# Performance work log

Measured on AMD Instinct MI355X. Metric: run time of the kernel, lower is better.

The kernel has to match this reference:

```python
import jax, jax.numpy as jnp
import numpy as np

N = 3072
FEAT = 128
E = 24576


def setup_inputs() -> dict:
    key = jax.random.key(0)
    k1, k2, k3, k4 = jax.random.split(key, 4)
    x = jax.random.normal(k1, (N, FEAT), dtype=jnp.float32)
    edge_index = jax.random.randint(k2, (2, E), 0, N, dtype=jnp.int32)
    batch = jnp.zeros((N,), dtype=jnp.int32)
    # lin: Linear(2*FEAT, 1)
    w = jax.random.normal(k3, (2 * FEAT,), dtype=jnp.float32) / np.sqrt(2 * FEAT)
    b = jax.random.normal(k4, (), dtype=jnp.float32) * 0.01
    return {"x": x, "edge_index": edge_index, "batch": batch, "w": w, "b": b}


def _cc_labels(adj):
    """Connected-component labels via min-label propagation + pointer jumping.
    Labels equal the minimum node index of each component, so ranking them by
    value reproduces scipy's first-occurrence component ordering."""
    n = adj.shape[0]
    adj = jax.lax.stop_gradient(adj)

    def body(state):
        labels, _ = state
        neigh = jnp.where(adj > 0, labels[None, :], n).min(axis=1)  # [n]
        new = jnp.minimum(labels, neigh)
        new = jnp.minimum(new, new[new])  # pointer jumping
        return new, jnp.any(new != labels)

    labels, _ = jax.lax.while_loop(lambda s: s[1], body,
                                   (jnp.arange(n), jnp.array(True)))
    return labels


def reference(x, edge_index, batch, w, b):
    n, f = x.shape
    idx = jnp.arange(n)
    src, dst = edge_index[0], edge_index[1]
    # undirected: duplicate each edge in both directions (coalesce in the
    # original dedups; dense scatter-set below is equivalent since duplicate
    # (u,v) edges get identical scores)
    s2 = jnp.concatenate([src, dst])
    d2 = jnp.concatenate([dst, src])
    # per-edge raw score: lin(concat(x[u], x[v]))  ->  tanh
    e = jnp.tanh(x[s2] @ w[:f] + x[d2] @ w[f:] + b)  # [2E]

    zero = jnp.zeros((n, n), dtype=x.dtype)
    A = zero.at[s2, d2].set(1.0).at[idx, idx].set(0.0)   # self-loops removed
    S = zero.at[s2, d2].set(e).at[idx, idx].set(0.0)
    contract = (e > 0.0).astype(x.dtype)                 # tanh -> threshold 0
    A_c = zero.at[s2, d2].max(contract).at[idx, idx].set(0.0)

    labels = _cc_labels(A_c)                             # min-node-index labels
    roots = (labels == idx).astype(jnp.int32)
    cluster = (jnp.cumsum(roots) - 1)[labels]            # consecutive 0..K-1
    C = jax.nn.one_hot(cluster, n, dtype=x.dtype)        # [n, n] (padded to n)

    single = (A_c.sum(axis=1) + A_c.sum(axis=0)) == 0    # isolated under contraction
    S = S.at[idx, idx].set(single.astype(x.dtype))

    X_new = (S @ C).T @ x                                # [n(padK), f]
    A_new = (C.T @ A @ C).at[idx, idx].set(0.0)          # dense coarsened adjacency
    new_batch = jnp.zeros((n,), dtype=batch.dtype).at[cluster].max(batch)
    return X_new, A_new, new_batch, cluster
```

## Files before the change

kernel.cpp:

```cpp
#include <hip/hip_runtime.h>
#include <math.h>

#define N 3072
#define FEAT 128
#define NE 24576
#define PSTRIDE 64
#define DOTB 768
#define OUTZ4 2458368
#define ZB3 608
#define GATB 192
#define RESCAP 4096

__device__ __forceinline__ void wave_agg_add(bool valid, int key, float val,
                                             float* base, int stride, int off) {
    int lane = threadIdx.x & 63;
    unsigned long long active = __ballot(valid ? 1 : 0);
    while (active) {
        int leader = __ffsll(active) - 1;
        int lkey = __shfl(key, leader);
        bool mine = valid && (key == lkey);
        unsigned long long grp = __ballot(mine ? 1 : 0);
        float v = mine ? val : 0.0f;
        #pragma unroll
        for (int o = 32; o; o >>= 1) v += __shfl_xor(v, o);
        if (lane == leader)
            atomicAdd(&base[(size_t)lkey * stride + off], v);
        active &= ~grp;
    }
}

__global__ void k_init(const float* __restrict__ x, const float* __restrict__ w,
                       float* __restrict__ a, float* __restrict__ c,
                       float4* __restrict__ zws) {
    int b = blockIdx.x, t = threadIdx.x;
    if (b < DOTB) {
        int node = b * 4 + (t >> 6);
        int lane = t & 63;
        const float* xi = x + node * FEAT;
        float pa = xi[lane] * w[lane] + xi[lane + 64] * w[lane + 64];
        float pc = xi[lane] * w[FEAT + lane] + xi[lane + 64] * w[FEAT + lane + 64];
        for (int off = 32; off; off >>= 1) {
            pa += __shfl_down(pa, off);
            pc += __shfl_down(pc, off);
        }
        if (lane == 0) { a[node] = pa; c[node] = pc; }
    } else {
        float4 z = {0.f, 0.f, 0.f, 0.f};
        #pragma unroll
        for (int k = 0; k < 6; ++k) zws[k * 256 + t] = z;
    }
}

__global__ void k_edge_pairs(const int* __restrict__ ei, const float* __restrict__ a,
                             const float* __restrict__ c, const float* __restrict__ bb,
                             unsigned* __restrict__ ep, int* __restrict__ notsingle,
                             int* __restrict__ pcnt, unsigned long long* __restrict__ ptab) {
    int t = blockIdx.x * blockDim.x + threadIdx.x;
    if (t >= NE) return;
    int u = ei[t], v = ei[NE + t];
    unsigned wpk = (unsigned)u | ((unsigned)v << 12);
    if (u != v) {
        float b = bb[0];
        float su = a[u] + c[v] + b;
        float sv = a[v] + c[u] + b;
        unsigned fu = (su > 0.f) ? 1u : 0u;
        unsigned fv = (sv > 0.f) ? 1u : 0u;
        wpk |= (fu << 24) | (fv << 25);
        if (fu | fv) { notsingle[u] = 1; notsingle[v] = 1; }
        float eu = tanhf(su);
        int sl = atomicAdd(&pcnt[v], 1);
        if (sl < PSTRIDE)
            ptab[(size_t)v * PSTRIDE + sl] =
                ((unsigned long long)__float_as_uint(eu) << 32) | (unsigned)u;
        float ev2 = tanhf(sv);
        sl = atomicAdd(&pcnt[u], 1);
        if (sl < PSTRIDE)
            ptab[(size_t)u * PSTRIDE + sl] =
                ((unsigned long long)__float_as_uint(ev2) << 32) | (unsigned)v;
    }
    ep[t] = wpk;
}

__global__ void __launch_bounds__(1024)
k_prop_gather(const unsigned* __restrict__ ep, const float* __restrict__ x,
              const int* __restrict__ pcnt, const unsigned long long* __restrict__ ptab,
              const int* __restrict__ notsingle, float* __restrict__ y,
              unsigned long long* __restrict__ qmask, int* __restrict__ cluster,
              float* __restrict__ out_cluster, float4* __restrict__ zout) {
    __shared__ int lab[N];
    __shared__ unsigned Vw[N / 32];
    __shared__ unsigned res[RESCAP];
    __shared__ unsigned short rnodes[N];
    __shared__ int ssum[1024];
    __shared__ unsigned short rk[N];
    __shared__ int sh_p[16 * 64];
    __shared__ int flag, rescnt, rncnt;
    int t = threadIdx.x, blk = blockIdx.x;
    int wv = t >> 6, lane = t & 63;
    if (blk == 0) {
        if (t < N / 32) Vw[t] = (t == 0) ? 1u : 0u;
        if (t == 0) { rescnt = 0; rncnt = 0; }
        unsigned act = 0x00FFFFFFu;
        for (;;) {
            __syncthreads();
            if (t == 0) flag = 0;
            __syncthreads();
            unsigned rem = act;
            while (rem) {
                int j = __ffs(rem) - 1;
                rem &= rem - 1;
                unsigned wpk = ep[t + j * 1024];
                if (!(wpk & 0x3000000u)) { act &= ~(1u << j); continue; }
                int u = wpk & 0xFFF, v = (wpk >> 12) & 0xFFF;
                unsigned pu = (Vw[u >> 5] >> (u & 31)) & 1u;
                unsigned pv = (Vw[v >> 5] >> (v & 31)) & 1u;
                if ((wpk & (1u << 24)) && pv && !pu) {
                    atomicOr(&Vw[u >> 5], 1u << (u & 31)); pu = 1; flag = 1;
                }
                if ((wpk & (1u << 25)) && pu && !pv) {
                    atomicOr(&Vw[v >> 5], 1u << (v & 31)); pv = 1; flag = 1;
                }
                bool done = (pu || !(wpk & (1u << 24))) && (pv || !(wpk & (1u << 25)));
                if (done) act &= ~(1u << j);
            }
            __syncthreads();
            if (!flag) break;
        }
        unsigned rem = act;
        while (rem) {
            int j = __ffs(rem) - 1;
            rem &= rem - 1;
            unsigned wpk = ep[t + j * 1024];
            int u = wpk & 0xFFF, v = (wpk >> 12) & 0xFFF;
            unsigned pu = (Vw[u >> 5] >> (u & 31)) & 1u;
            unsigned pv = (Vw[v >> 5] >> (v & 31)) & 1u;
            if ((wpk & (1u << 24)) && !pu) {
                int pos = atomicAdd(&rescnt, 1);
                if (pos < RESCAP) res[pos] = (unsigned)u | ((unsigned)v << 12);
            }
            if ((wpk & (1u << 25)) && !pv) {
                int pos = atomicAdd(&rescnt, 1);
                if (pos < RESCAP) res[pos] = (unsigned)v | ((unsigned)u << 12);
            }
        }
        for (int i = t; i < N; i += 1024) {
            unsigned inV = (Vw[i >> 5] >> (i & 31)) & 1u;
            lab[i] = inV ? 0 : i;
            if (!inV) {
                int pos = atomicAdd(&rncnt, 1);
                rnodes[pos] = (unsigned short)i;
            }
        }
        __syncthreads();
        int nres = rescnt < RESCAP ? rescnt : RESCAP;
        bool ovf = (rescnt > RESCAP);
        int nrn = rncnt;
        for (;;) {
            __syncthreads();
            if (t == 0) flag = 0;
            __syncthreads();
            if (!ovf) {
                for (int k = t; k < nres; k += 1024) {
                    unsigned w2 = res[k];
                    int p = w2 & 0xFFF, q = (w2 >> 12) & 0xFFF;
                    int lq = lab[q];
                    if (lq < lab[p]) { atomicMin(&lab[p], lq); flag = 1; }
                }
                for (int k = t; k < nrn; k += 1024) {
                    int i = rnodes[k];
                    int m = lab[i];
                    int mm = lab[m];
                    while (mm < m) { m = mm; mm = lab[m]; }
                    if (m < lab[i]) { atomicMin(&lab[i], m); flag = 1; }
                }
            } else {
                for (int j = 0; j < 24; ++j) {
                    unsigned wpk = ep[t + j * 1024];
                    int u = wpk & 0xFFF, v = (wpk >> 12) & 0xFFF;
                    if (wpk & (1u << 24)) {
                        int lv = lab[v];
                        if (lv < lab[u]) { atomicMin(&lab[u], lv); flag = 1; }
                    }
                    if (wpk & (1u << 25)) {
                        int lu = lab[u];
                        if (lu < lab[v]) { atomicMin(&lab[v], lu); flag = 1; }
                    }
                }
                for (int i = t; i < N; i += 1024) {
                    int m = lab[i];
                    if (m == 0) continue;
                    int mm = lab[m];
                    while (mm < m) { m = mm; mm = lab[m]; }
                    if (m < lab[i]) { atomicMin(&lab[i], m); flag = 1; }
                }
            }
            __syncthreads();
            if (!flag) break;
        }
        int i0 = 3 * t;
        int r0 = (lab[i0] == i0);
        int r1 = (lab[i0 + 1] == i0 + 1);
        int r2 = (lab[i0 + 2] == i0 + 2);
        int s = r0 + r1 + r2;
        ssum[t] = s;
        __syncthreads();
        for (int off = 1; off < 1024; off <<= 1) {
            int val = (t >= off) ? ssum[t - off] : 0;
            __syncthreads();
            ssum[t] += val;
            __syncthreads();
        }
        int run = ssum[t] - s;
        run += r0; rk[i0]     = (unsigned short)(run - 1);
        run += r1; rk[i0 + 1] = (unsigned short)(run - 1);
        run += r2; rk[i0 + 2] = (unsigned short)(run - 1);
        __syncthreads();
        for (int j = t; j < N; j += 1024) {
            int cl = rk[lab[j]];
            cluster[j] = cl;
            out_cluster[j] = (float)cl;
        }
    } else if (blk <= GATB) {
        int q = (blk - 1) * 16 + wv;
        int cnt = pcnt[q]; if (cnt > PSTRIDE) cnt = PSTRIDE;
        const unsigned long long* row = ptab + (size_t)q * PSTRIDE;
        int myp = -1 - lane;
        float mye = 0.f;
        if (lane < cnt) {
            unsigned long long s = row[lane];
            myp = (int)(s & 0xFFFFFFFFu);
            mye = __uint_as_float((unsigned)(s >> 32));
        }
        sh_p[wv * 64 + lane] = myp;
        bool dup = false;
        for (int j = 0; j < lane && !dup; ++j)
            dup = (sh_p[wv * 64 + j] == myp);
        bool valid = (lane < cnt) && !dup;
        unsigned long long m = __ballot(valid ? 1 : 0);
        if (lane == 0) qmask[q] = m;
        float acc0 = 0.f, acc1 = 0.f;
        for (int j = 0; j < cnt; ++j) {
            if (!((m >> j) & 1ull)) continue;
            int p = __shfl(myp, j);
            float e = __shfl(mye, j);
            const float* xp = x + p * FEAT;
            acc0 += e * xp[lane];
            acc1 += e * xp[lane + 64];
        }
        if (!notsingle[q]) {
            const float* xq = x + q * FEAT;
            acc0 += xq[lane];
            acc1 += xq[lane + 64];
        }
        float* yq = y + q * FEAT;
        yq[lane] = acc0;
        yq[lane + 64] = acc1;
    } else {
        float4 z = {0.f, 0.f, 0.f, 0.f};
        int base = (blk - GATB - 1) * 4096;
        #pragma unroll
        for (int k = 0; k < 4; ++k) {
            int idx = base + k * 1024 + t;
            if (idx < OUTZ4) zout[idx] = z;
        }
    }
}

__global__ void k_reduce_anew(const float* __restrict__ y, const int* __restrict__ cluster,
                              const int* __restrict__ pcnt,
                              const unsigned long long* __restrict__ ptab,
                              const unsigned long long* __restrict__ qmask,
                              float* __restrict__ Xnew, float* __restrict__ Anew) {
    int gid = blockIdx.x * blockDim.x + threadIdx.x;
    int wid = gid >> 6, lane = gid & 63;
    if (wid < 6144) {
        int f = wid & (FEAT - 1);
        int chunk = wid >> 7;
        int q = chunk * 64 + lane;
        wave_agg_add(true, cluster[q], y[q * FEAT + f], Xnew, FEAT, f);
    } else {
        int q = wid - 6144;
        int cnt = pcnt[q]; if (cnt > PSTRIDE) cnt = PSTRIDE;
        unsigned long long m = qmask[q];
        bool valid = (lane < cnt) && ((m >> lane) & 1ull);
        int p = 0;
        if (valid) p = (int)(ptab[(size_t)q * PSTRIDE + lane] & 0xFFFFFFFFu);
        int cq = cluster[q];
        int cp = valid ? cluster[p] : 0;
        valid = valid && (cp != cq);
        wave_agg_add(valid, cp * N + cq, 1.0f, Anew, 1, 0);
    }
}

extern "C" void kernel_launch(void* const* d_in, const int* in_sizes, int n_in,
                              void* d_out, int out_size, void* d_ws, size_t ws_size,
                              hipStream_t stream) {
    const float* x  = (const float*)d_in[0];
    const int*   ei = (const int*)d_in[1];
    const float* w  = (const float*)d_in[3];
    const float* bb = (const float*)d_in[4];

    char* ws = (char*)d_ws;
    size_t off = 0;
    int* pcnt     = (int*)(ws + off);      off += (size_t)N * 4;
    int* notsing  = (int*)(ws + off);      off += (size_t)N * 4;
    float* a      = (float*)(ws + off);    off += (size_t)N * 4;
    float* c      = (float*)(ws + off);    off += (size_t)N * 4;
    int* cluster  = (int*)(ws + off);      off += (size_t)N * 4;
    unsigned* ep  = (unsigned*)(ws + off); off += (size_t)NE * 4;
    unsigned long long* qmask = (unsigned long long*)(ws + off); off += (size_t)N * 8;
    float* y      = (float*)(ws + off);    off += (size_t)N * FEAT * 4;
    unsigned long long* ptab = (unsigned long long*)(ws + off); off += (size_t)N * PSTRIDE * 8;

    float* Xnew        = (float*)d_out;
    float* Anew        = Xnew + (size_t)N * FEAT;
    float* out_cluster = Anew + (size_t)N * N + N;

    k_init<<<DOTB + 1, 256, 0, stream>>>(x, w, a, c, (float4*)pcnt);
    k_edge_pairs<<<NE / 256, 256, 0, stream>>>(ei, a, c, bb, ep, notsing, pcnt, ptab);
    k_prop_gather<<<1 + GATB + ZB3, 1024, 0, stream>>>(ep, x, pcnt, ptab, notsing, y,
                                                       qmask, cluster, out_cluster,
                                                       (float4*)d_out);
    k_reduce_anew<<<(9216 * 64) / 1024, 1024, 0, stream>>>(y, cluster, pcnt, ptab,
                                                           qmask, Xnew, Anew);
}
```

Baseline: 134.0 us.

## Fuse gather and reduction kernels using in-kernel spin-wait barriers

Merges the feature-gather and the Xnew/Anew scatter-reduction into a single launch. Gather blocks keep their per-node aggregates in registers and wait on global counters until the cluster labels are computed and the output buffers are zeroed. Before issuing atomics they combine same-cluster rows within the block through shared memory. This removes the y and qmask round-trip through global memory and one kernel launch. In exchange it relies on all 770 blocks of 1024 threads being co-resident, which risks deadlock or serialization if they are not.

Result: slower. 387.4 us (+189.2%).

```diff
diff --git a/kernel.cpp b/kernel.cpp
--- a/kernel.cpp
+++ b/kernel.cpp
@@ -6,9 +6,9 @@
 #define NE 24576
 #define PSTRIDE 64
 #define DOTB 768
-#define OUTZ4 2458368
-#define ZB3 608
 #define GATB 192
+#define AZ4 2360064
+#define AZB 577
 #define RESCAP 4096
 
 __device__ __forceinline__ void wave_agg_add(bool valid, int key, float val,
@@ -29,6 +29,10 @@
     }
 }
 
+__device__ __forceinline__ int ctrl_ld(const int* p) {
+    return __hip_atomic_load(p, __ATOMIC_RELAXED, __HIP_MEMORY_SCOPE_AGENT);
+}
+
 __global__ void k_init(const float* __restrict__ x, const float* __restrict__ w,
                        float* __restrict__ a, float* __restrict__ c,
                        float4* __restrict__ zws) {
@@ -47,7 +51,10 @@
     } else {
         float4 z = {0.f, 0.f, 0.f, 0.f};
         #pragma unroll
-        for (int k = 0; k < 6; ++k) zws[k * 256 + t] = z;
+        for (int k = 0; k < 7; ++k) {
+            int idx = k * 256 + t;
+            if (idx < 1540) zws[idx] = z;
+        }
     }
 }
 
@@ -82,11 +89,11 @@
 }
 
 __global__ void __launch_bounds__(1024)
-k_prop_gather(const unsigned* __restrict__ ep, const float* __restrict__ x,
-              const int* __restrict__ pcnt, const unsigned long long* __restrict__ ptab,
-              const int* __restrict__ notsingle, float* __restrict__ y,
-              unsigned long long* __restrict__ qmask, int* __restrict__ cluster,
-              float* __restrict__ out_cluster, float4* __restrict__ zout) {
+k_pgr2(const unsigned* __restrict__ ep, const float* __restrict__ x,
+       const int* __restrict__ pcnt, const unsigned long long* __restrict__ ptab,
+       const int* __restrict__ notsingle, int* __restrict__ cluster,
+       float* __restrict__ out_cluster, float* __restrict__ Xnew,
+       float* __restrict__ Anew, int* __restrict__ ctrl) {
     __shared__ int lab[N];
     __shared__ unsigned Vw[N / 32];
     __shared__ unsigned res[RESCAP];
@@ -94,6 +101,9 @@
     __shared__ int ssum[1024];
     __shared__ unsigned short rk[N];
     __shared__ int sh_p[16 * 64];
+    __shared__ int sh_cq[16];
+    __shared__ float sh_a0[16 * 64];
+    __shared__ float sh_a1[16 * 64];
     __shared__ int flag, rescnt, rncnt;
     int t = threadIdx.x, blk = blockIdx.x;
     int wv = t >> 6, lane = t & 63;
@@ -220,7 +230,17 @@
             cluster[j] = cl;
             out_cluster[j] = (float)cl;
         }
+        __syncthreads();
+        __threadfence();
+        if (t == 0) atomicAdd(&ctrl[2], 1);
     } else if (blk <= GATB) {
+        {
+            float4 z = {0.f, 0.f, 0.f, 0.f};
+            if (t < 512) ((float4*)Xnew)[(blk - 1) * 512 + t] = z;
+            __syncthreads();
+            __threadfence();
+            if (t == 0) atomicAdd(&ctrl[4], 1);
+        }
         int q = (blk - 1) * 16 + wv;
         int cnt = pcnt[q]; if (cnt > PSTRIDE) cnt = PSTRIDE;
         const unsigned long long* row = ptab + (size_t)q * PSTRIDE;
@@ -237,7 +257,6 @@
             dup = (sh_p[wv * 64 + j] == myp);
         bool valid = (lane < cnt) && !dup;
         unsigned long long m = __ballot(valid ? 1 : 0);
-        if (lane == 0) qmask[q] = m;
         float acc0 = 0.f, acc1 = 0.f;
         for (int j = 0; j < cnt; ++j) {
             if (!((m >> j) & 1ull)) continue;
@@ -252,43 +271,43 @@
             acc0 += xq[lane];
             acc1 += xq[lane + 64];
         }
-        float* yq = y + q * FEAT;
-        yq[lane] = acc0;
-        yq[lane + 64] = acc1;
+        if (t == 0) {
+            while (ctrl_ld(&ctrl[4]) < GATB) __builtin_amdgcn_s_sleep(2);
+            while (ctrl_ld(&ctrl[2]) < 1)    __builtin_amdgcn_s_sleep(2);
+            while (ctrl_ld(&ctrl[3]) < AZB)  __builtin_amdgcn_s_sleep(2);
+        }
+        __syncthreads();
+        __threadfence();
+        int cq = cluster[q];
+        if (lane == 0) sh_cq[wv] = cq;
+        sh_a0[wv * 64 + lane] = acc0;
+        sh_a1[wv * 64 + lane] = acc1;
+        __syncthreads();
+        bool leader = true;
+        for (int j = 0; j < wv; ++j)
+            if (sh_cq[j] == cq) leader = false;
+        if (leader) {
+            float s0 = acc0, s1 = acc1;
+            for (int j = wv + 1; j < 16; ++j)
+                if (sh_cq[j] == cq) { s0 += sh_a0[j * 64 + lane]; s1 += sh_a1[j * 64 + lane]; }
+            atomicAdd(&Xnew[cq * FEAT + lane], s0);
+            atomicAdd(&Xnew[cq * FEAT + 64 + lane], s1);
+        }
+        int cp = valid ? cluster[myp] : 0;
+        bool av = valid && (cp != cq);
+        wave_agg_add(av, cp * N + cq, 1.0f, Anew, 1, 0);
     } else {
         float4 z = {0.f, 0.f, 0.f, 0.f};
+        float4* az = (float4*)Anew;
         int base = (blk - GATB - 1) * 4096;
         #pragma unroll
         for (int k = 0; k < 4; ++k) {
             int idx = base + k * 1024 + t;
-            if (idx < OUTZ4) zout[idx] = z;
-        }
-    }
-}
-
-__global__ void k_reduce_anew(const float* __restrict__ y, const int* __restrict__ cluster,
-                              const int* __restrict__ pcnt,
-                              const unsigned long long* __restrict__ ptab,
-                              const unsigned long long* __restrict__ qmask,
-                              float* __restrict__ Xnew, float* __restrict__ Anew) {
-    int gid = blockIdx.x * blockDim.x + threadIdx.x;
-    int wid = gid >> 6, lane = gid & 63;
-    if (wid < 6144) {
-        int f = wid & (FEAT - 1);
-        int chunk = wid >> 7;
-        int q = chunk * 64 + lane;
-        wave_agg_add(true, cluster[q], y[q * FEAT + f], Xnew, FEAT, f);
-    } else {
-        int q = wid - 6144;
-        int cnt = pcnt[q]; if (cnt > PSTRIDE) cnt = PSTRIDE;
-        unsigned long long m = qmask[q];
-        bool valid = (lane < cnt) && ((m >> lane) & 1ull);
-        int p = 0;
-        if (valid) p = (int)(ptab[(size_t)q * PSTRIDE + lane] & 0xFFFFFFFFu);
-        int cq = cluster[q];
-        int cp = valid ? cluster[p] : 0;
-        valid = valid && (cp != cq);
-        wave_agg_add(valid, cp * N + cq, 1.0f, Anew, 1, 0);
+            if (idx < AZ4) az[idx] = z;
+        }
+        __syncthreads();
+        __threadfence();
+        if (t == 0) atomicAdd(&ctrl[3], 1);
     }
 }
 
@@ -302,25 +321,21 @@
 
     char* ws = (char*)d_ws;
     size_t off = 0;
+    int* ctrl     = (int*)(ws + off);      off += 64;
     int* pcnt     = (int*)(ws + off);      off += (size_t)N * 4;
     int* notsing  = (int*)(ws + off);      off += (size_t)N * 4;
     float* a      = (float*)(ws + off);    off += (size_t)N * 4;
     float* c      = (float*)(ws + off);    off += (size_t)N * 4;
     int* cluster  = (int*)(ws + off);      off += (size_t)N * 4;
     unsigned* ep  = (unsigned*)(ws + off); off += (size_t)NE * 4;
-    unsigned long long* qmask = (unsigned long long*)(ws + off); off += (size_t)N * 8;
-    float* y      = (float*)(ws + off);    off += (size_t)N * FEAT * 4;
     unsigned long long* ptab = (unsigned long long*)(ws + off); off += (size_t)N * PSTRIDE * 8;
 
     float* Xnew        = (float*)d_out;
     float* Anew        = Xnew + (size_t)N * FEAT;
     float* out_cluster = Anew + (size_t)N * N + N;
 
-    k_init<<<DOTB + 1, 256, 0, stream>>>(x, w, a, c, (float4*)pcnt);
+    k_init<<<DOTB + 1, 256, 0, stream>>>(x, w, a, c, (float4*)ctrl);
     k_edge_pairs<<<NE / 256, 256, 0, stream>>>(ei, a, c, bb, ep, notsing, pcnt, ptab);
-    k_prop_gather<<<1 + GATB + ZB3, 1024, 0, stream>>>(ep, x, pcnt, ptab, notsing, y,
-                                                       qmask, cluster, out_cluster,
-                                                       (float4*)d_out);
-    k_reduce_anew<<<(9216 * 64) / 1024, 1024, 0, stream>>>(y, cluster, pcnt, ptab,
-                                                           qmask, Xnew, Anew);
-}
+    k_pgr2<<<1 + GATB + AZB, 1024, 0, stream>>>(ep, x, pcnt, ptab, notsing,
+                                                cluster, out_cluster, Xnew, Anew, ctrl);
+}
```

## Fuse edge, propagation and reduction kernels into persistent kernel with grid barriers

Applied to the files above, without the earlier changes.

Merges the edge-pair, propagation/gather and reduce kernels into one 256-block persistent kernel separated by software grid barriers. The output zeroing moves into the init kernel, which also clears the barrier counters. This removes two kernel launches and their gaps. In exchange, every block now waits at the barriers for the single-block label propagation, and correctness relies on all 256 blocks of 1024 threads being resident at the same time.

New measurement: 177.4 us. 1.32x slower.

```diff
diff --git a/kernel.cpp b/kernel.cpp
--- a/kernel.cpp
+++ b/kernel.cpp
@@ -6,9 +6,9 @@
 #define NE 24576
 #define PSTRIDE 64
 #define DOTB 768
-#define OUTZ4 2458368
-#define ZB3 608
-#define GATB 192
+#define OZ4 2459136
+#define OZB 2402
+#define NBLK 256
 #define RESCAP 4096
 
 __device__ __forceinline__ void wave_agg_add(bool valid, int key, float val,
@@ -29,9 +29,30 @@
     }
 }
 
+__device__ __forceinline__ void gsync(int* bar, int* lgen) {
+    __syncthreads();
+    if (threadIdx.x == 0) {
+        __threadfence();
+        int g = ++(*lgen);
+        if (atomicAdd(&bar[0], 1) == (int)gridDim.x - 1) {
+            __hip_atomic_store(&bar[0], 0, __ATOMIC_RELAXED, __HIP_MEMORY_SCOPE_AGENT);
+            __threadfence();
+            atomicAdd(&bar[1], 1);
+        } else {
+            while (__hip_atomic_load(&bar[1], __ATOMIC_RELAXED,
+                                     __HIP_MEMORY_SCOPE_AGENT) < g)
+                __builtin_amdgcn_s_sleep(8);
+        }
+        __threadfence();
+    } else {
+        ++(*lgen);
+    }
+    __syncthreads();
+}
+
 __global__ void k_init(const float* __restrict__ x, const float* __restrict__ w,
                        float* __restrict__ a, float* __restrict__ c,
-                       float4* __restrict__ zws) {
+                       float4* __restrict__ zout, float4* __restrict__ zws) {
     int b = blockIdx.x, t = threadIdx.x;
     if (b < DOTB) {
         int node = b * 4 + (t >> 6);
@@ -44,49 +65,33 @@
             pc += __shfl_down(pc, off);
         }
         if (lane == 0) { a[node] = pa; c[node] = pc; }
+    } else if (b < DOTB + OZB) {
+        float4 z = {0.f, 0.f, 0.f, 0.f};
+        int base = (b - DOTB) * 1024;
+        #pragma unroll
+        for (int k = 0; k < 4; ++k) {
+            int idx = base + k * 256 + t;
+            if (idx < OZ4) zout[idx] = z;
+        }
     } else {
         float4 z = {0.f, 0.f, 0.f, 0.f};
         #pragma unroll
-        for (int k = 0; k < 6; ++k) zws[k * 256 + t] = z;
-    }
-}
-
-__global__ void k_edge_pairs(const int* __restrict__ ei, const float* __restrict__ a,
-                             const float* __restrict__ c, const float* __restrict__ bb,
-                             unsigned* __restrict__ ep, int* __restrict__ notsingle,
-                             int* __restrict__ pcnt, unsigned long long* __restrict__ ptab) {
-    int t = blockIdx.x * blockDim.x + threadIdx.x;
-    if (t >= NE) return;
-    int u = ei[t], v = ei[NE + t];
-    unsigned wpk = (unsigned)u | ((unsigned)v << 12);
-    if (u != v) {
-        float b = bb[0];
-        float su = a[u] + c[v] + b;
-        float sv = a[v] + c[u] + b;
-        unsigned fu = (su > 0.f) ? 1u : 0u;
-        unsigned fv = (sv > 0.f) ? 1u : 0u;
-        wpk |= (fu << 24) | (fv << 25);
-        if (fu | fv) { notsingle[u] = 1; notsingle[v] = 1; }
-        float eu = tanhf(su);
-        int sl = atomicAdd(&pcnt[v], 1);
-        if (sl < PSTRIDE)
-            ptab[(size_t)v * PSTRIDE + sl] =
-                ((unsigned long long)__float_as_uint(eu) << 32) | (unsigned)u;
-        float ev2 = tanhf(sv);
-        sl = atomicAdd(&pcnt[u], 1);
-        if (sl < PSTRIDE)
-            ptab[(size_t)u * PSTRIDE + sl] =
-                ((unsigned long long)__float_as_uint(ev2) << 32) | (unsigned)v;
-    }
-    ep[t] = wpk;
+        for (int k = 0; k < 7; ++k) {
+            int idx = k * 256 + t;
+            if (idx < 1540) zws[idx] = z;
+        }
+    }
 }
 
 __global__ void __launch_bounds__(1024)
-k_prop_gather(const unsigned* __restrict__ ep, const float* __restrict__ x,
-              const int* __restrict__ pcnt, const unsigned long long* __restrict__ ptab,
-              const int* __restrict__ notsingle, float* __restrict__ y,
-              unsigned long long* __restrict__ qmask, int* __restrict__ cluster,
-              float* __restrict__ out_cluster, float4* __restrict__ zout) {
+k_mega2(const int* __restrict__ ei, const float* __restrict__ x,
+        const float* __restrict__ a, const float* __restrict__ c,
+        const float* __restrict__ bb, int* __restrict__ bar,
+        int* __restrict__ pcnt, int* __restrict__ notsingle,
+        unsigned* __restrict__ ep, unsigned long long* __restrict__ ptab,
+        unsigned long long* __restrict__ qmask, float* __restrict__ y,
+        int* __restrict__ cluster, float* __restrict__ out_cluster,
+        float* __restrict__ Xnew, float* __restrict__ Anew) {
     __shared__ int lab[N];
     __shared__ unsigned Vw[N / 32];
     __shared__ unsigned res[RESCAP];
@@ -97,6 +102,35 @@
     __shared__ int flag, rescnt, rncnt;
     int t = threadIdx.x, blk = blockIdx.x;
     int wv = t >> 6, lane = t & 63;
+    int lgen = 0;
+
+    if (t < 96) {
+        int s = blk * 96 + t;
+        int u = ei[s], v = ei[NE + s];
+        unsigned wpk = (unsigned)u | ((unsigned)v << 12);
+        if (u != v) {
+            float b = bb[0];
+            float su = a[u] + c[v] + b;
+            float sv = a[v] + c[u] + b;
+            unsigned fu = (su > 0.f) ? 1u : 0u;
+            unsigned fv = (sv > 0.f) ? 1u : 0u;
+            wpk |= (fu << 24) | (fv << 25);
+            if (fu | fv) { notsingle[u] = 1; notsingle[v] = 1; }
+            float eu = tanhf(su);
+            int sl = atomicAdd(&pcnt[v], 1);
+            if (sl < PSTRIDE)
+                ptab[(size_t)v * PSTRIDE + sl] =
+                    ((unsigned long long)__float_as_uint(eu) << 32) | (unsigned)u;
+            float ev2 = tanhf(sv);
+            sl = atomicAdd(&pcnt[u], 1);
+            if (sl < PSTRIDE)
+                ptab[(size_t)u * PSTRIDE + sl] =
+                    ((unsigned long long)__float_as_uint(ev2) << 32) | (unsigned)v;
+        }
+        ep[s] = wpk;
+    }
+    gsync(bar, &lgen);
+
     if (blk == 0) {
         if (t < N / 32) Vw[t] = (t == 0) ? 1u : 0u;
         if (t == 0) { rescnt = 0; rncnt = 0; }
@@ -220,7 +254,7 @@
             cluster[j] = cl;
             out_cluster[j] = (float)cl;
         }
-    } else if (blk <= GATB) {
+    } else if (blk <= 192) {
         int q = (blk - 1) * 16 + wv;
         int cnt = pcnt[q]; if (cnt > PSTRIDE) cnt = PSTRIDE;
         const unsigned long long* row = ptab + (size_t)q * PSTRIDE;
@@ -255,40 +289,27 @@
         float* yq = y + q * FEAT;
         yq[lane] = acc0;
         yq[lane + 64] = acc1;
-    } else {
-        float4 z = {0.f, 0.f, 0.f, 0.f};
-        int base = (blk - GATB - 1) * 4096;
-        #pragma unroll
-        for (int k = 0; k < 4; ++k) {
-            int idx = base + k * 1024 + t;
-            if (idx < OUTZ4) zout[idx] = z;
-        }
-    }
-}
-
-__global__ void k_reduce_anew(const float* __restrict__ y, const int* __restrict__ cluster,
-                              const int* __restrict__ pcnt,
-                              const unsigned long long* __restrict__ ptab,
-                              const unsigned long long* __restrict__ qmask,
-                              float* __restrict__ Xnew, float* __restrict__ Anew) {
-    int gid = blockIdx.x * blockDim.x + threadIdx.x;
-    int wid = gid >> 6, lane = gid & 63;
-    if (wid < 6144) {
-        int f = wid & (FEAT - 1);
-        int chunk = wid >> 7;
-        int q = chunk * 64 + lane;
-        wave_agg_add(true, cluster[q], y[q * FEAT + f], Xnew, FEAT, f);
-    } else {
-        int q = wid - 6144;
-        int cnt = pcnt[q]; if (cnt > PSTRIDE) cnt = PSTRIDE;
-        unsigned long long m = qmask[q];
-        bool valid = (lane < cnt) && ((m >> lane) & 1ull);
-        int p = 0;
-        if (valid) p = (int)(ptab[(size_t)q * PSTRIDE + lane] & 0xFFFFFFFFu);
-        int cq = cluster[q];
-        int cp = valid ? cluster[p] : 0;
-        valid = valid && (cp != cq);
-        wave_agg_add(valid, cp * N + cq, 1.0f, Anew, 1, 0);
+    }
+    gsync(bar, &lgen);
+
+    for (int gw = blk * 16 + wv; gw < 9216; gw += NBLK * 16) {
+        if (gw < 6144) {
+            int f = gw & (FEAT - 1);
+            int chunk = gw >> 7;
+            int q = chunk * 64 + lane;
+            wave_agg_add(true, cluster[q], y[q * FEAT + f], Xnew, FEAT, f);
+        } else {
+            int q = gw - 6144;
+            int cnt = pcnt[q]; if (cnt > PSTRIDE) cnt = PSTRIDE;
+            unsigned long long m = qmask[q];
+            bool valid = (lane < cnt) && ((m >> lane) & 1ull);
+            int p = 0;
+            if (valid) p = (int)(ptab[(size_t)q * PSTRIDE + lane] & 0xFFFFFFFFu);
+            int cq = cluster[q];
+            int cp = valid ? cluster[p] : 0;
+            valid = valid && (cp != cq);
+            wave_agg_add(valid, cp * N + cq, 1.0f, Anew, 1, 0);
+        }
     }
 }
 
@@ -302,6 +323,7 @@
 
     char* ws = (char*)d_ws;
     size_t off = 0;
+    int* bar      = (int*)(ws + off);      off += 64;
     int* pcnt     = (int*)(ws + off);      off += (size_t)N * 4;
     int* notsing  = (int*)(ws + off);      off += (size_t)N * 4;
     float* a      = (float*)(ws + off);    off += (size_t)N * 4;
@@ -316,11 +338,9 @@
     float* Anew        = Xnew + (size_t)N * FEAT;
     float* out_cluster = Anew + (size_t)N * N + N;
 
-    k_init<<<DOTB + 1, 256, 0, stream>>>(x, w, a, c, (float4*)pcnt);
-    k_edge_pairs<<<NE / 256, 256, 0, stream>>>(ei, a, c, bb, ep, notsing, pcnt, ptab);
-    k_prop_gather<<<1 + GATB + ZB3, 1024, 0, stream>>>(ep, x, pcnt, ptab, notsing, y,
-                                                       qmask, cluster, out_cluster,
-                                                       (float4*)d_out);
-    k_reduce_anew<<<(9216 * 64) / 1024, 1024, 0, stream>>>(y, cluster, pcnt, ptab,
-                                                           qmask, Xnew, Anew);
-}
+    k_init<<<DOTB + OZB + 1, 256, 0, stream>>>(x, w, a, c,
+                                               (float4*)d_out, (float4*)bar);
+    k_mega2<<<NBLK, 1024, 0, stream>>>(ei, x, a, c, bb, bar, pcnt, notsing,
+                                       ep, ptab, qmask, y, cluster,
+                                       out_cluster, Xnew, Anew);
+}
```
